# Performance work log

Hardware: AMD Instinct MI355X
Metric: run time of the kernel (lower is better)

Reference implementation:

```python
import jax, jax.numpy as jnp
import numpy as np

DN = ('NCDHW', 'OIDHW', 'NCDHW')

def conv(x, w, stride=1):
    k = w.shape[-1]
    pad = 'VALID' if k == 2 else 'SAME'  # ks=2,s=2 Minkowski offsets {0,1}; ks=3 centered; ks=1 pointwise
    return jax.lax.conv_general_dilated(x, w, (stride,) * 3, pad, dimension_numbers=DN)

def masked_bn(x, m, eps=1e-5):
    # BatchNorm over occupied voxels only (MinkowskiBatchNorm semantics); affine is identity at init.
    cnt = jnp.maximum(jnp.sum(m), 1.0)
    mean = jnp.sum(x * m, axis=(0, 2, 3, 4)) / cnt
    xc = (x - mean.reshape(1, -1, 1, 1, 1)) * m  # also zeroes unoccupied sites
    var = jnp.sum(xc * xc, axis=(0, 2, 3, 4)) / cnt
    return xc * jax.lax.rsqrt(var + eps).reshape(1, -1, 1, 1, 1)

def downmask(m):
    B, _, D, H, W = m.shape
    return m.reshape(B, 1, D // 2, 2, H // 2, 2, W // 2, 2).max(axis=(3, 5, 7))

def cbr(x, m, w):
    return jax.nn.relu(masked_bn(conv(x, w), m))

def res(x, m, wa, wb, wsk):
    y = masked_bn(conv(jax.nn.relu(masked_bn(conv(x, wa), m)), wb), m)
    sk = x if wsk is None else masked_bn(conv(x, wsk), m)
    return jax.nn.relu(y + sk)

def stage(x, m, wd, wa1, wb1, wsk, wa2, wb2):
    m2 = downmask(m)  # output coord set of ks=2,s=2 sparse conv
    x = jax.nn.relu(masked_bn(conv(x, wd, 2), m2))  # BasicConvolutionBlock
    x = res(x, m2, wa1, wb1, wsk)
    x = res(x, m2, wa2, wb2, None)
    return x, m2

def _forward(feats, mask, ws0, ws1, d1, a11, b11, a12, b12, d2, a21, b21, k2, a22, b22,
             d3, a31, b31, k3, a32, b32, d4, a41, b41, k4, a42, b42):
    m = mask
    x = cbr(feats * m, m, ws0)
    x = cbr(x, m, ws1)
    x, m = stage(x, m, d1, a11, b11, None, a12, b12)   # 32 -> 32 (identity skip)
    x, m = stage(x, m, d2, a21, b21, k2, a22, b22)     # 32 -> 64
    x, m = stage(x, m, d3, a31, b31, k3, a32, b32)     # 64 -> 128
    x, m = stage(x, m, d4, a41, b41, k4, a42, b42)     # 128 -> 256
    return x

def setup_inputs() -> dict:
    key = jax.random.key(0)
    ks = jax.random.split(key, 28)
    def W(k, o, i, s):
        return jax.random.normal(k, (o, i, s, s, s), jnp.float32) / np.sqrt(i * s ** 3)
    feats = jax.random.normal(ks[0], (2, 3, 64, 64, 64), jnp.float32)
    mask = (jax.random.uniform(ks[1], (2, 1, 64, 64, 64)) < 0.1).astype(jnp.float32)
    return dict(
        feats=feats * mask, mask=mask,
        ws0=W(ks[2], 32, 3, 3), ws1=W(ks[3], 32, 32, 3),
        d1=W(ks[4], 32, 32, 2), a11=W(ks[5], 32, 32, 3), b11=W(ks[6], 32, 32, 3),
        a12=W(ks[7], 32, 32, 3), b12=W(ks[8], 32, 32, 3),
        d2=W(ks[9], 32, 32, 2), a21=W(ks[10], 64, 32, 3), b21=W(ks[11], 64, 64, 3),
        k2=W(ks[12], 64, 32, 1), a22=W(ks[13], 64, 64, 3), b22=W(ks[14], 64, 64, 3),
        d3=W(ks[15], 64, 64, 2), a31=W(ks[16], 128, 64, 3), b31=W(ks[17], 128, 128, 3),
        k3=W(ks[18], 128, 64, 1), a32=W(ks[19], 128, 128, 3), b32=W(ks[20], 128, 128, 3),
        d4=W(ks[21], 128, 128, 2), a41=W(ks[22], 256, 128, 3), b41=W(ks[23], 256, 256, 3),
        k4=W(ks[24], 256, 128, 1), a42=W(ks[25], 256, 256, 3), b42=W(ks[26], 256, 256, 3))

def reference(feats, mask, ws0, ws1, d1, a11, b11, a12, b12, d2, a21, b21, k2, a22, b22,
              d3, a31, b31, k3, a32, b32, d4, a41, b41, k4, a42, b42):
    return _forward(feats, mask, ws0, ws1, d1, a11, b11, a12, b12, d2, a21, b21, k2, a22, b22,
                    d3, a31, b31, k3, a32, b32, d4, a41, b41, k4, a42, b42)
```

## Files before the change

### kernel.cpp

```cpp
#include <hip/hip_runtime.h>

#define BLK 256

static inline int gup(long work) { return (int)((work + BLK - 1) / BLK); }

__device__ inline bool occ_pred(const float* mask, const int* fmap,
                                int i, int DHW, int Ho, int Wo, int mode) {
  if (mode == 0) return mask[i] > 0.f;
  int b = i / DHW, sp = i - b * DHW;
  int HW = Ho * Wo;
  int z = sp / HW, r = sp - z * HW, y = r / Wo, x = r - y * Wo;
  int Hi = 2 * Ho, Wi = 2 * Wo;
  const int* mb = fmap + b * 8 * DHW;
  int base = ((2 * z) * Hi + 2 * y) * Wi + 2 * x;
  bool occ = false;
  for (int dz = 0; dz < 2; dz++)
    for (int dy = 0; dy < 2; dy++)
      for (int dx = 0; dx < 2; dx++)
        occ |= mb[base + dz * Hi * Wi + dy * Wi + dx] >= 0;
  return occ;
}

__global__ __launch_bounds__(1024) void cnt_k(const float* mask, const int* fmap,
    int* bcnt, int DHW, int Ho, int Wo, int mode, int total) {
  int i = blockIdx.x * 1024 + threadIdx.x;
  bool occ = (i < total) && occ_pred(mask, fmap, i, DHW, Ho, Wo, mode);
  unsigned long long bal = __ballot(occ);
  __shared__ int ws[16];
  int lane = threadIdx.x & 63, wid = threadIdx.x >> 6;
  if (lane == 0) ws[wid] = __popcll(bal);
  __syncthreads();
  if (threadIdx.x == 0) {
    int a = 0;
    for (int w = 0; w < 16; w++) a += ws[w];
    bcnt[blockIdx.x] = a;
  }
}

__global__ __launch_bounds__(1024) void scan_k(int* bcnt, int nb, int* cnt) {
  __shared__ int sh[1024];
  int t = threadIdx.x;
  int v = (t < nb) ? bcnt[t] : 0;
  sh[t] = v;
  __syncthreads();
  for (int o = 1; o < 1024; o <<= 1) {
    int u = (t >= o) ? sh[t - o] : 0;
    __syncthreads();
    sh[t] += u;
    __syncthreads();
  }
  if (t < nb) bcnt[t] = sh[t] - v;
  if (t == 0) *cnt = sh[1023];
}

__global__ __launch_bounds__(1024) void emit_k(const float* mask, const int* fmap,
    const int* boff, int* map, int* list, int DHW, int Ho, int Wo, int mode, int total) {
  int i = blockIdx.x * 1024 + threadIdx.x;
  bool occ = (i < total) && occ_pred(mask, fmap, i, DHW, Ho, Wo, mode);
  unsigned long long bal = __ballot(occ);
  int lane = threadIdx.x & 63, wid = threadIdx.x >> 6;
  __shared__ int wcnt[16], woff[16];
  if (lane == 0) wcnt[wid] = __popcll(bal);
  __syncthreads();
  if (threadIdx.x == 0) {
    int a = boff[blockIdx.x];
    for (int w = 0; w < 16; w++) { woff[w] = a; a += wcnt[w]; }
  }
  __syncthreads();
  if (i < total) {
    if (occ) {
      int p = woff[wid] + __popcll(bal & ((1ull << lane) - 1ull));
      map[i] = p; list[p] = i;
    } else map[i] = -1;
  }
}

__global__ __launch_bounds__(1024) void compact1_k(const int* __restrict__ fmap,
    int* __restrict__ map, int* __restrict__ list, int* __restrict__ cntp,
    int Do, int Ho, int Wo) {
  int DHW = Do * Ho * Wo, total = 2 * DHW;
  int tid = threadIdx.x, lane = tid & 63, wid = tid >> 6;
  bool occ = (tid < total) && occ_pred(nullptr, fmap, tid, DHW, Ho, Wo, 1);
  unsigned long long bal = __ballot(occ);
  __shared__ int wcnt[16], woff[16];
  if (lane == 0) wcnt[wid] = __popcll(bal);
  __syncthreads();
  if (tid == 0) {
    int a = 0;
    for (int w = 0; w < 16; w++) { woff[w] = a; a += wcnt[w]; }
    *cntp = a;
  }
  __syncthreads();
  if (tid < total) {
    if (occ) {
      int p = woff[wid] + __popcll(bal & ((1ull << lane) - 1ull));
      map[tid] = p; list[p] = tid;
    } else map[tid] = -1;
  }
}

__global__ __launch_bounds__(256) void csr_both_k(
    const int* __restrict__ list, const int* __restrict__ map,
    const int* __restrict__ cntp, const int* __restrict__ fmap,
    int* __restrict__ csr27, int* __restrict__ csr8,
    int D, int H, int W, int do8) {
  int n = *cntp;
  int DHW = D * H * W;
  for (int v = blockIdx.x * 256 + threadIdx.x; v < n; v += gridDim.x * 256) {
    int idx = list[v];
    int b = idx / DHW, sp = idx - b * DHW;
    int z = sp / (H * W), r = sp - z * H * W, y = r / W, x = r - y * W;
    const int* mb = map + b * DHW;
    int* e = csr27 + (long)v * 28;
    int cnt = 0;
    for (int k = 0; k < 27; k++) {
      int dz = k / 9 - 1, dy = (k / 3) % 3 - 1, dx = k % 3 - 1;
      int zz = z + dz, yy = y + dy, xx = x + dx;
      if ((unsigned)zz >= (unsigned)D || (unsigned)yy >= (unsigned)H ||
          (unsigned)xx >= (unsigned)W) continue;
      int j = mb[(zz * H + yy) * W + xx];
      if (j >= 0) e[++cnt] = (k << 24) | j;
    }
    e[0] = cnt;
    for (int s = cnt + 1; s <= 27; s++) e[s] = -1;
    if (do8) {
      int Hi = 2 * H, Wi = 2 * W;
      const int* fb = fmap + b * 8 * DHW;
      int* e8 = csr8 + (long)v * 9;
      int c8 = 0;
      for (int k = 0; k < 8; k++) {
        int dz = k >> 2, dy = (k >> 1) & 1, dx = k & 1;
        int j = fb[((2 * z + dz) * Hi + 2 * y + dy) * Wi + 2 * x + dx];
        if (j >= 0) e8[++c8] = (k << 24) | j;
      }
      e8[0] = c8;
      for (int s = c8 + 1; s <= 8; s++) e8[s] = -1;
    }
  }
}

struct WAll {
  const float* src[25];
  float* dst[25];
  int O[25], I[25], K[25];
  int sb[26];
};

__global__ __launch_bounds__(256) void wtr_all_k(WAll wa) {
  int b = blockIdx.x;
  int w = 0;
  while (w < 24 && b >= wa.sb[w + 1]) ++w;
  int O = wa.O[w], I = wa.I[w], K = wa.K[w];
  int I4 = (I + 3) >> 2;
  long tot = (long)K * I4 * O * 4;
  long t = (long)(b - wa.sb[w]) * 256 + threadIdx.x;
  if (t >= tot) return;
  int e = (int)(t & 3); long r = t >> 2;
  int co = (int)(r % O); long r2 = r / O;
  int ci4 = (int)(r2 % I4); int k = (int)(r2 / I4);
  int ci = 4 * ci4 + e;
  wa.dst[w][t] = (ci < I) ? wa.src[w][((long)co * I + ci) * K + k] : 0.f;
}

__global__ void gather0_k(const float* __restrict__ feats, const int* __restrict__ list,
                          const int* __restrict__ cntp, float* __restrict__ rows, int DHW) {
  int n = *cntp;
  int t = blockIdx.x * BLK + threadIdx.x;
  if (t >= n * 4) return;
  int vox = t >> 2, c = t & 3;
  int idx = list[vox]; int b = idx / DHW, sp = idx - b * DHW;
  rows[t] = (c < 3) ? feats[(b * 3 + c) * DHW + sp] : 0.f;
}

template <int CIN, int COUT, int CPT, int VX, int NT, bool PRE>
__global__ __launch_bounds__(256) void convk_k(
    const float* __restrict__ fin, const float* __restrict__ wt,
    float* __restrict__ fout, const int* __restrict__ csr,
    const int* __restrict__ cntp, const int* __restrict__ pcntp,
    const float* __restrict__ pslot, float* __restrict__ slot) {
  constexpr int CL = COUT / CPT;
  constexpr int G = 256 / CL;
  constexpr int VT = G * VX;
  constexpr int C4 = CIN / 4;
  constexpr int WSZ = C4 * COUT;
  __shared__ int jtab[VT * NT];
  __shared__ float4 rbuf[VT * C4];
  __shared__ float4 wbuf[WSZ];
  __shared__ float aP[PRE ? CIN : 4], bP[PRE ? CIN : 4];
  __shared__ float swA[256], swB[256];
  int n = *cntp;
  int vb = blockIdx.x * VT;
  if (vb >= n) return;
  int tid = threadIdx.x;
  if constexpr (PRE) {
    int np = *pcntp;
    float c = fmaxf((float)np, 1.f);
    for (int ch = tid; ch < CIN; ch += 256) {
      float s = 0.f, q = 0.f;
      #pragma unroll
      for (int r = 0; r < 4; r++) { s += pslot[r * 512 + ch]; q += pslot[r * 512 + 256 + ch]; }
      float mean = s / c, var = fmaxf(q / c - mean * mean, 0.f);
      float a = rsqrtf(var + 1e-5f);
      aP[ch] = a; bP[ch] = -mean * a;
    }
  }
  for (int u = tid; u < VT * NT; u += 256) jtab[u] = -1;
  __syncthreads();
  for (int u = tid; u < VT * (NT + 1); u += 256) {
    int v = u / (NT + 1), s = u - v * (NT + 1);
    if (s > 0 && vb + v < n) {
      int e = csr[(long)(vb + v) * (NT + 1) + s];
      if (e >= 0) jtab[v * NT + (e >> 24)] = e & 0xFFFFFF;
    }
  }
  int cl = tid % CL, g = tid / CL, vg = g * VX;
  float acc[VX][CPT];
  #pragma unroll
  for (int vx = 0; vx < VX; vx++)
    #pragma unroll
    for (int m = 0; m < CPT; m++) acc[vx][m] = 0.f;
  const float4* fin4 = (const float4*)fin;
  const float4* w4 = (const float4*)wt;
  for (int k = 0; k < NT; k++) {
    __syncthreads();
    for (int u = tid; u < WSZ; u += 256) wbuf[u] = w4[(long)k * WSZ + u];
    for (int u = tid; u < VT * C4; u += 256) {
      int v = u / C4, c4 = u - v * C4;
      int j = jtab[v * NT + k];
      float4 val = make_float4(0.f, 0.f, 0.f, 0.f);
      if (j >= 0) {
        val = fin4[(long)j * C4 + c4];
        if constexpr (PRE) {
          int ch = 4 * c4;
          val.x = fmaxf(val.x * aP[ch] + bP[ch], 0.f);
          val.y = fmaxf(val.y * aP[ch + 1] + bP[ch + 1], 0.f);
          val.z = fmaxf(val.z * aP[ch + 2] + bP[ch + 2], 0.f);
          val.w = fmaxf(val.w * aP[ch + 3] + bP[ch + 3], 0.f);
        }
      }
      rbuf[u] = val;
    }
    __syncthreads();
    #pragma unroll
    for (int c4 = 0; c4 < C4; c4++) {
      float4 w_[CPT];
      #pragma unroll
      for (int m = 0; m < CPT; m++) w_[m] = wbuf[c4 * COUT + cl + m * CL];
      #pragma unroll
      for (int vx = 0; vx < VX; vx++) {
        float4 rv = rbuf[(vg + vx) * C4 + c4];
        #pragma unroll
        for (int m = 0; m < CPT; m++)
          acc[vx][m] += rv.x * w_[m].x + rv.y * w_[m].y + rv.z * w_[m].z + rv.w * w_[m].w;
      }
    }
  }
  #pragma unroll
  for (int vx = 0; vx < VX; vx++) {
    int v = vb + vg + vx;
    if (v < n) {
      #pragma unroll
      for (int m = 0; m < CPT; m++)
        fout[(long)v * COUT + cl + m * CL] = acc[vx][m];
    }
  }
  int lane = tid & 63, wid = tid >> 6;
  #pragma unroll
  for (int m = 0; m < CPT; m++) {
    float ps = 0.f, pq = 0.f;
    #pragma unroll
    for (int vx = 0; vx < VX; vx++) { ps += acc[vx][m]; pq += acc[vx][m] * acc[vx][m]; }
    #pragma unroll
    for (int o = 32; o >= CL; o >>= 1) {
      ps += __shfl_down(ps, o);
      pq += __shfl_down(pq, o);
    }
    if (lane < CL) {
      swA[(m * 4 + wid) * CL + lane] = ps;
      swB[(m * 4 + wid) * CL + lane] = pq;
    }
  }
  __syncthreads();
  if (tid < COUT) {
    int m = tid / CL, c2 = tid % CL;
    float s = 0.f, q = 0.f;
    #pragma unroll
    for (int w = 0; w < 4; w++) {
      s += swA[(m * 4 + w) * CL + c2];
      q += swB[(m * 4 + w) * CL + c2];
    }
    float* sl = slot + (blockIdx.x & 3) * 512;
    atomicAdd(&sl[tid], s);
    atomicAdd(&sl[256 + tid], q);
  }
}

template <int CIN, int COUT, int ES, bool PRE>
__global__ __launch_bounds__(256) void convc_k(
    const float* __restrict__ fin, const float* __restrict__ wt,
    float* __restrict__ fout, const int* __restrict__ csr,
    const int* __restrict__ cntp, const int* __restrict__ pcntp,
    const float* __restrict__ pslot, float* __restrict__ slot) {
  constexpr int CL = COUT / 2, G = 256 / CL, C4 = CIN / 4;
  constexpr int EST = (ES > 0) ? ES : 1;
  constexpr int CPD = PRE ? CIN : 4;
  __shared__ float4 rbuf[G * C4];
  __shared__ int se[G * EST];
  __shared__ float aP[CPD], bP[CPD];
  __shared__ float sA[256], sB[256];
  __shared__ int scmax;
  int n = *cntp;
  int vb = blockIdx.x * G;
  if (vb >= n) return;
  int tid = threadIdx.x;
  if constexpr (PRE) {
    int np = *pcntp;
    float c = fmaxf((float)np, 1.f);
    for (int ch = tid; ch < CIN; ch += 256) {
      float s = 0.f, q = 0.f;
      #pragma unroll
      for (int r = 0; r < 4; r++) { s += pslot[r * 512 + ch]; q += pslot[r * 512 + 256 + ch]; }
      float mean = s / c, var = fmaxf(q / c - mean * mean, 0.f);
      float a = rsqrtf(var + 1e-5f);
      aP[ch] = a; bP[ch] = -mean * a;
    }
  }
  int cmax;
  if constexpr (ES > 0) {
    if (tid == 0) scmax = 0;
    __syncthreads();
    for (int u = tid; u < G * ES; u += 256) {
      int v = vb + u / ES;
      int e = (v < n) ? csr[(long)vb * ES + u] : 0;
      se[u] = e;
      if ((u % ES) == 0) atomicMax(&scmax, e);
    }
    __syncthreads();
    cmax = scmax;
  } else {
    __syncthreads();
    cmax = 1;
  }
  int cl = tid % CL, g = tid / CL;
  int v = vb + g;
  bool alive = v < n;
  float a0 = 0.f, a1 = 0.f;
  const float4* fin4 = (const float4*)fin;
  const float4* w4 = (const float4*)wt;
  for (int i = 1; i <= cmax; i++) {
    __syncthreads();
    for (int u = tid; u < G * C4; u += 256) {
      int gg = u / C4, c4 = u - gg * C4;
      int pj = -1;
      if constexpr (ES > 0) {
        if (vb + gg < n && i <= se[gg * EST]) pj = se[gg * EST + i];
      } else {
        if (vb + gg < n) pj = vb + gg;
      }
      float4 val = make_float4(0.f, 0.f, 0.f, 0.f);
      if (pj >= 0) {
        int j = pj & 0xFFFFFF;
        val = fin4[(long)j * C4 + c4];
        if constexpr (PRE) {
          int ch = 4 * c4;
          val.x = fmaxf(val.x * aP[ch] + bP[ch], 0.f);
          val.y = fmaxf(val.y * aP[ch + 1] + bP[ch + 1], 0.f);
          val.z = fmaxf(val.z * aP[ch + 2] + bP[ch + 2], 0.f);
          val.w = fmaxf(val.w * aP[ch + 3] + bP[ch + 3], 0.f);
        }
      }
      rbuf[u] = val;
    }
    __syncthreads();
    int pj;
    if constexpr (ES > 0) {
      pj = (alive && i <= se[g * EST]) ? se[g * EST + i] : -1;
    } else {
      pj = alive ? v : -1;
    }
    if (pj >= 0) {
      int k = pj >> 24;
      const float4* wk = w4 + (long)k * C4 * COUT + cl;
      #pragma unroll 8
      for (int c4 = 0; c4 < C4; c4++) {
        float4 rv = rbuf[g * C4 + c4];
        float4 w0 = wk[c4 * COUT];
        float4 w1 = wk[c4 * COUT + CL];
        a0 += rv.x * w0.x + rv.y * w0.y + rv.z * w0.z + rv.w * w0.w;
        a1 += rv.x * w1.x + rv.y * w1.y + rv.z * w1.z + rv.w * w1.w;
      }
    }
  }
  if (alive) {
    fout[(long)v * COUT + cl] = a0;
    fout[(long)v * COUT + cl + CL] = a1;
  }
  __syncthreads();
  sA[tid] = alive ? a0 : 0.f; sB[tid] = alive ? a1 : 0.f;
  __syncthreads();
  for (int o = 128; o >= CL; o >>= 1) {
    if (tid < o) { sA[tid] += sA[tid + o]; sB[tid] += sB[tid + o]; }
    __syncthreads();
  }
  float s0 = 0.f, s1 = 0.f;
  if (tid < CL) { s0 = sA[tid]; s1 = sB[tid]; }
  __syncthreads();
  sA[tid] = alive ? a0 * a0 : 0.f; sB[tid] = alive ? a1 * a1 : 0.f;
  __syncthreads();
  for (int o = 128; o >= CL; o >>= 1) {
    if (tid < o) { sA[tid] += sA[tid + o]; sB[tid] += sB[tid + o]; }
    __syncthreads();
  }
  if (tid < CL) {
    float* sl = slot + (blockIdx.x & 3) * 512;
    atomicAdd(&sl[tid], s0);
    atomicAdd(&sl[tid + CL], s1);
    atomicAdd(&sl[256 + tid], sA[tid]);
    atomicAdd(&sl[256 + tid + CL], sB[tid]);
  }
}

template <int CIN, int COUT, int NS, bool PRE>
__global__ __launch_bounds__(256) void convs_k(
    const float* __restrict__ fin, const float* __restrict__ wt,
    float* __restrict__ fout, const int* __restrict__ csr,
    const int* __restrict__ cntp, const int* __restrict__ pcntp,
    const float* __restrict__ pslot) {
  constexpr int CL = COUT / 2, G = 256 / CL, C4 = CIN / 4;
  constexpr int CPD = PRE ? CIN : 4;
  __shared__ float4 rbuf[G * C4];
  __shared__ int se[G * 28];
  __shared__ float aP[CPD], bP[CPD];
  __shared__ int scmax;
  int n = *cntp;
  int vb = blockIdx.x * G;
  if (vb >= n) return;
  int tid = threadIdx.x;
  int y = blockIdx.y;
  if constexpr (PRE) {
    int np = *pcntp;
    float c = fmaxf((float)np, 1.f);
    for (int ch = tid; ch < CIN; ch += 256) {
      float s = 0.f, q = 0.f;
      #pragma unroll
      for (int r = 0; r < 4; r++) { s += pslot[r * 512 + ch]; q += pslot[r * 512 + 256 + ch]; }
      float mean = s / c, var = fmaxf(q / c - mean * mean, 0.f);
      float a = rsqrtf(var + 1e-5f);
      aP[ch] = a; bP[ch] = -mean * a;
    }
  }
  if (tid == 0) scmax = 0;
  __syncthreads();
  for (int u = tid; u < G * 28; u += 256) {
    int v = vb + u / 28;
    int e = (v < n) ? csr[(long)vb * 28 + u] : 0;
    se[u] = e;
    if ((u % 28) == 0) atomicMax(&scmax, e);
  }
  __syncthreads();
  int cmax = scmax;
  int cl = tid % CL, g = tid / CL;
  int v = vb + g;
  bool alive = v < n;
  float a0 = 0.f, a1 = 0.f;
  const float4* fin4 = (const float4*)fin;
  const float4* w4 = (const float4*)wt;
  for (int i = 1 + y; i <= cmax; i += NS) {
    __syncthreads();
    for (int u = tid; u < G * C4; u += 256) {
      int gg = u / C4, c4 = u - gg * C4;
      int pj = -1;
      if (vb + gg < n && i <= se[gg * 28]) pj = se[gg * 28 + i];
      float4 val = make_float4(0.f, 0.f, 0.f, 0.f);
      if (pj >= 0) {
        int j = pj & 0xFFFFFF;
        val = fin4[(long)j * C4 + c4];
        if constexpr (PRE) {
          int ch = 4 * c4;
          val.x = fmaxf(val.x * aP[ch] + bP[ch], 0.f);
          val.y = fmaxf(val.y * aP[ch + 1] + bP[ch + 1], 0.f);
          val.z = fmaxf(val.z * aP[ch + 2] + bP[ch + 2], 0.f);
          val.w = fmaxf(val.w * aP[ch + 3] + bP[ch + 3], 0.f);
        }
      }
      rbuf[u] = val;
    }
    __syncthreads();
    int pj = (alive && i <= se[g * 28]) ? se[g * 28 + i] : -1;
    if (pj >= 0) {
      int k = pj >> 24;
      const float4* wk = w4 + (long)k * C4 * COUT + cl;
      #pragma unroll 8
      for (int c4 = 0; c4 < C4; c4++) {
        float4 rv = rbuf[g * C4 + c4];
        float4 w0 = wk[c4 * COUT];
        float4 w1 = wk[c4 * COUT + CL];
        a0 += rv.x * w0.x + rv.y * w0.y + rv.z * w0.z + rv.w * w0.w;
        a1 += rv.x * w1.x + rv.y * w1.y + rv.z * w1.z + rv.w * w1.w;
      }
    }
  }
  if (alive) {
    atomicAdd(&fout[(long)v * COUT + cl], a0);
    atomicAdd(&fout[(long)v * COUT + cl + CL], a1);
  }
}

template <int C>
__global__ __launch_bounds__(BLK) void bnred_k(const float* __restrict__ rows,
    const int* __restrict__ cntp, float* __restrict__ slot) {
  int n = *cntp;
  long tot = (long)n * C;
  int tid = threadIdx.x;
  float s = 0.f, s2 = 0.f;
  for (long t = (long)blockIdx.x * BLK + tid; t < tot; t += (long)gridDim.x * BLK) {
    float v = rows[t]; s += v; s2 += v * v;
  }
  __shared__ float sh[BLK], sh2[BLK];
  sh[tid] = s; sh2[tid] = s2;
  __syncthreads();
  for (int o = BLK / 2; o >= C; o >>= 1) {
    if (tid < o) { sh[tid] += sh[tid + o]; sh2[tid] += sh2[tid + o]; }
    __syncthreads();
  }
  if (tid < C) { atomicAdd(&slot[tid], sh[tid]); atomicAdd(&slot[256 + tid], sh2[tid]); }
}

template <int C, int MODE>
__global__ __launch_bounds__(256) void skipapp_k(
    const float* __restrict__ x, const float* __restrict__ y,
    const float* __restrict__ s1, const float* __restrict__ s2,
    const int* __restrict__ cntp, float* __restrict__ out) {
  __shared__ float a1_[C], b1_[C], a2_[C], b2_[C];
  int n = *cntp;
  int tid = threadIdx.x;
  float cnt = fmaxf((float)n, 1.f);
  for (int c = tid; c < C; c += 256) {
    float s = 0.f, q = 0.f;
    #pragma unroll
    for (int r = 0; r < 4; r++) { s += s1[r * 512 + c]; q += s1[r * 512 + 256 + c]; }
    float mean = s / cnt, var = fmaxf(q / cnt - mean * mean, 0.f);
    float a = rsqrtf(var + 1e-5f);
    a1_[c] = a; b1_[c] = -mean * a;
    if (MODE != 2) {
      s = 0.f; q = 0.f;
      #pragma unroll
      for (int r = 0; r < 4; r++) { s += s2[r * 512 + c]; q += s2[r * 512 + 256 + c]; }
      mean = s / cnt; var = fmaxf(q / cnt - mean * mean, 0.f);
      a = rsqrtf(var + 1e-5f);
      a2_[c] = a; b2_[c] = -mean * a;
    }
  }
  __syncthreads();
  constexpr int C4 = C / 4;
  long tot = (long)n * C4;
  for (long t = (long)blockIdx.x * 256 + tid; t < tot; t += (long)gridDim.x * 256) {
    int c = 4 * (int)(t % C4);
    float4 xv = ((const float4*)x)[t];
    float4 yv = ((const float4*)y)[t];
    float4 o;
    o.x = xv.x * a1_[c] + b1_[c];
    o.y = xv.y * a1_[c + 1] + b1_[c + 1];
    o.z = xv.z * a1_[c + 2] + b1_[c + 2];
    o.w = xv.w * a1_[c + 3] + b1_[c + 3];
    if (MODE == 0) {
      o.x += yv.x * a2_[c] + b2_[c];
      o.y += yv.y * a2_[c + 1] + b2_[c + 1];
      o.z += yv.z * a2_[c + 2] + b2_[c + 2];
      o.w += yv.w * a2_[c + 3] + b2_[c + 3];
    } else if (MODE == 1) {
      o.x += fmaxf(yv.x * a2_[c] + b2_[c], 0.f);
      o.y += fmaxf(yv.y * a2_[c + 1] + b2_[c + 1], 0.f);
      o.z += fmaxf(yv.z * a2_[c + 2] + b2_[c + 2], 0.f);
      o.w += fmaxf(yv.w * a2_[c + 3] + b2_[c + 3], 0.f);
    } else {
      o.x += yv.x; o.y += yv.y; o.z += yv.z; o.w += yv.w;
    }
    o.x = fmaxf(o.x, 0.f); o.y = fmaxf(o.y, 0.f);
    o.z = fmaxf(o.z, 0.f); o.w = fmaxf(o.w, 0.f);
    ((float4*)out)[t] = o;
  }
}

__global__ void scatter_k(const float* __restrict__ rows, const int* __restrict__ list,
                          const int* __restrict__ cntp, float* __restrict__ out, int DHW) {
  int n = *cntp;
  int t = blockIdx.x * BLK + threadIdx.x;
  if (t >= n * 256) return;
  int vox = t >> 8, c = t & 255;
  int idx = list[vox]; int b = idx / DHW, sp = idx - b * DHW;
  out[(b * 256 + c) * DHW + sp] = rows[t];
}

#define CAP0 81920
#define CAP1 57344
#define CAP2 8192
#define CAP3 1024
#define CAP4 128

extern "C" void kernel_launch(void* const* d_in, const int* in_sizes, int n_in,
                              void* d_out, int out_size, void* d_ws, size_t ws_size,
                              hipStream_t stream) {
  const float* feats = (const float*)d_in[0];
  const float* mask0 = (const float*)d_in[1];

  char* p = (char*)d_ws;
  auto alloc = [&](size_t bytes) { char* r = p; p += (bytes + 255) & ~255ull; return r; };

  const int tab[25][4] = {
    {2, 32, 3, 27},  {3, 32, 32, 27}, {4, 32, 32, 8},  {5, 32, 32, 27}, {6, 32, 32, 27},
    {7, 32, 32, 27}, {8, 32, 32, 27}, {9, 32, 32, 8},  {10, 64, 32, 27},{11, 64, 64, 27},
    {12, 64, 32, 1}, {13, 64, 64, 27},{14, 64, 64, 27},{15, 64, 64, 8}, {16, 128, 64, 27},
    {17, 128, 128, 27},{18, 128, 64, 1},{19, 128, 128, 27},{20, 128, 128, 27},
    {21, 128, 128, 8},{22, 256, 128, 27},{23, 256, 256, 27},{24, 256, 128, 1},
    {25, 256, 256, 27},{26, 256, 256, 27},
  };
  WAll wa;
  float* wT[27] = {nullptr};
  int blk = 0;
  for (int i = 0; i < 25; i++) {
    int idx = tab[i][0], O = tab[i][1], I = tab[i][2], K = tab[i][3];
    int I4 = (I + 3) / 4;
    long sz = (long)K * I4 * O * 4;
    wT[idx] = (float*)alloc((size_t)sz * 4);
    wa.src[i] = (const float*)d_in[idx]; wa.dst[i] = wT[idx];
    wa.O[i] = O; wa.I[i] = I; wa.K[i] = K;
    wa.sb[i] = blk; blk += (int)((sz + 255) / 256);
  }
  wa.sb[25] = blk;

  int* map0 = (int*)alloc(524288 * 4);
  int* list0 = (int*)alloc((size_t)CAP0 * 4);
  int* map1 = (int*)alloc(65536 * 4);
  int* list1 = (int*)alloc((size_t)CAP1 * 4);
  int* map2 = (int*)alloc(8192 * 4);
  int* list2 = (int*)alloc(8192 * 4);
  int* map3 = (int*)alloc(1024 * 4);
  int* list3 = (int*)alloc(1024 * 4);
  int* map4 = (int*)alloc(128 * 4);
  int* list4 = (int*)alloc(128 * 4);
  int* bcnt = (int*)alloc(1024 * 4);
  int* cnts = (int*)alloc(32 * 4);
  int* c27_0 = (int*)alloc((size_t)CAP0 * 28 * 4);
  int* c27_1 = (int*)alloc((size_t)CAP1 * 28 * 4);
  int* c8_1  = (int*)alloc((size_t)CAP1 * 9 * 4);
  int* c27_2 = (int*)alloc((size_t)CAP2 * 28 * 4);
  int* c8_2  = (int*)alloc((size_t)CAP2 * 9 * 4);
  int* c27_3 = (int*)alloc((size_t)CAP3 * 28 * 4);
  int* c8_3  = (int*)alloc((size_t)CAP3 * 9 * 4);
  int* c27_4 = (int*)alloc((size_t)CAP4 * 28 * 4);
  int* c8_4  = (int*)alloc((size_t)CAP4 * 9 * 4);
  float* stats = (float*)alloc(25 * 2048 * 4);
  float* G0  = (float*)alloc((size_t)CAP0 * 4 * 4);
  float* F0a = (float*)alloc((size_t)CAP0 * 32 * 4);
  float* F0b = (float*)alloc((size_t)CAP0 * 32 * 4);
  float *R1[4], *R2[4];
  for (int i = 0; i < 4; i++) R1[i] = (float*)alloc((size_t)CAP1 * 32 * 4);
  for (int i = 0; i < 4; i++) R2[i] = (float*)alloc((size_t)CAP2 * 64 * 4);
  size_t z3sz = (size_t)CAP3 * 128 * 4 * 6 + (size_t)CAP4 * 256 * 4 * 6;
  float* Z3 = (float*)alloc(z3sz);
  float* R3[6], *R4[6];
  for (int i = 0; i < 6; i++) R3[i] = Z3 + (size_t)i * CAP3 * 128;
  for (int i = 0; i < 6; i++) R4[i] = Z3 + (size_t)6 * CAP3 * 128 + (size_t)i * CAP4 * 256;

  hipMemsetAsync(stats, 0, 25 * 2048 * 4, stream);
  hipMemsetAsync(Z3, 0, z3sz, stream);
  hipMemsetAsync(d_out, 0, (size_t)out_size * 4, stream);

  wtr_all_k<<<blk, 256, 0, stream>>>(wa);

  int* n0 = cnts + 0; int* n1 = cnts + 1; int* n2 = cnts + 2;
  int* n3 = cnts + 3; int* n4 = cnts + 4;

  cnt_k<<<512, 1024, 0, stream>>>(mask0, nullptr, bcnt, 262144, 64, 64, 0, 524288);
  scan_k<<<1, 1024, 0, stream>>>(bcnt, 512, n0);
  emit_k<<<512, 1024, 0, stream>>>(mask0, nullptr, bcnt, map0, list0, 262144, 64, 64, 0, 524288);
  gather0_k<<<gup((long)CAP0 * 4), BLK, 0, stream>>>(feats, list0, n0, G0, 262144);
  csr_both_k<<<512, 256, 0, stream>>>(list0, map0, n0, nullptr, c27_0, nullptr, 64, 64, 64, 0);

  cnt_k<<<64, 1024, 0, stream>>>(nullptr, map0, bcnt, 32768, 32, 32, 1, 65536);
  scan_k<<<1, 1024, 0, stream>>>(bcnt, 64, n1);
  emit_k<<<64, 1024, 0, stream>>>(nullptr, map0, bcnt, map1, list1, 32768, 32, 32, 1, 65536);
  csr_both_k<<<256, 256, 0, stream>>>(list1, map1, n1, map0, c27_1, c8_1, 32, 32, 32, 1);

  cnt_k<<<8, 1024, 0, stream>>>(nullptr, map1, bcnt, 4096, 16, 16, 1, 8192);
  scan_k<<<1, 1024, 0, stream>>>(bcnt, 8, n2);
  emit_k<<<8, 1024, 0, stream>>>(nullptr, map1, bcnt, map2, list2, 4096, 16, 16, 1, 8192);
  csr_both_k<<<32, 256, 0, stream>>>(list2, map2, n2, map1, c27_2, c8_2, 16, 16, 16, 1);

  compact1_k<<<1, 1024, 0, stream>>>(map2, map3, list3, n3, 8, 8, 8);
  csr_both_k<<<4, 256, 0, stream>>>(list3, map3, n3, map2, c27_3, c8_3, 8, 8, 8, 1);

  compact1_k<<<1, 1024, 0, stream>>>(map3, map4, list4, n4, 4, 4, 4);
  csr_both_k<<<1, 256, 0, stream>>>(list4, map4, n4, map3, c27_4, c8_4, 4, 4, 4, 1);

  auto slot = [&](int i) { return stats + (size_t)i * 2048; };
  auto bgrid = [&](long cap, int C) { long g = (cap * C / 4 + 255) / 256; return (int)(g > 2048 ? 2048 : g); };

  {
    int g = (CAP0 + 63) / 64;
    convk_k<4, 32, 4, 2, 27, false><<<g, 256, 0, stream>>>(G0, wT[2], F0a, c27_0, n0, nullptr, nullptr, slot(0));
    convk_k<32, 32, 4, 2, 27, true><<<g, 256, 0, stream>>>(F0a, wT[3], F0b, c27_0, n0, n0, slot(0), slot(1));
  }

  {
    int g = (CAP1 + 63) / 64, ag = bgrid(CAP1, 32);
    convk_k<32, 32, 4, 2, 8, true><<<g, 256, 0, stream>>>(F0b, wT[4], R1[0], c8_1, n1, n0, slot(1), slot(2));
    convk_k<32, 32, 4, 2, 27, true><<<g, 256, 0, stream>>>(R1[0], wT[5], R1[1], c27_1, n1, n1, slot(2), slot(3));
    convk_k<32, 32, 4, 2, 27, true><<<g, 256, 0, stream>>>(R1[1], wT[6], R1[2], c27_1, n1, n1, slot(3), slot(4));
    skipapp_k<32, 1><<<ag, 256, 0, stream>>>(R1[2], R1[0], slot(4), slot(2), n1, R1[3]);
    convk_k<32, 32, 4, 2, 27, false><<<g, 256, 0, stream>>>(R1[3], wT[7], R1[1], c27_1, n1, nullptr, nullptr, slot(5));
    convk_k<32, 32, 4, 2, 27, true><<<g, 256, 0, stream>>>(R1[1], wT[8], R1[2], c27_1, n1, n1, slot(5), slot(6));
    skipapp_k<32, 2><<<ag, 256, 0, stream>>>(R1[2], R1[3], slot(6), nullptr, n1, R1[0]);
  }

  {
    int g32 = (CAP2 + 31) / 32, ag = bgrid(CAP2, 64);
    convk_k<32, 32, 4, 1, 8, false><<<g32, 256, 0, stream>>>(R1[0], wT[9], R2[0], c8_2, n2, nullptr, nullptr, slot(7));
    convk_k<32, 64, 4, 2, 27, true><<<g32, 256, 0, stream>>>(R2[0], wT[10], R2[1], c27_2, n2, n2, slot(7), slot(8));
    convk_k<64, 64, 4, 2, 27, true><<<g32, 256, 0, stream>>>(R2[1], wT[11], R2[2], c27_2, n2, n2, slot(8), slot(9));
    convc_k<32, 64, 0, true><<<(CAP2 + 7) / 8, 256, 0, stream>>>(R2[0], wT[12], R2[3], nullptr, n2, n2, slot(7), slot(10));
    skipapp_k<64, 0><<<ag, 256, 0, stream>>>(R2[2], R2[3], slot(9), slot(10), n2, R2[1]);
    convk_k<64, 64, 4, 2, 27, false><<<g32, 256, 0, stream>>>(R2[1], wT[13], R2[0], c27_2, n2, nullptr, nullptr, slot(11));
    convk_k<64, 64, 4, 2, 27, true><<<g32, 256, 0, stream>>>(R2[0], wT[14], R2[2], c27_2, n2, n2, slot(11), slot(12));
    skipapp_k<64, 2><<<ag, 256, 0, stream>>>(R2[2], R2[1], slot(12), nullptr, n2, R2[3]);
  }

  {
    int gP = (CAP3 + 7) / 8, gO = (CAP3 + 3) / 4, ag = bgrid(CAP3, 128);
    int rO = gup((long)CAP3 * 128); if (rO > 512) rO = 512;
    convc_k<64, 64, 9, false><<<gP, 256, 0, stream>>>(R2[3], wT[15], R3[0], c8_3, n3, nullptr, nullptr, slot(13));
    convs_k<64, 128, 4, true><<<dim3(gO, 4), 256, 0, stream>>>(R3[0], wT[16], R3[1], c27_3, n3, n3, slot(13));
    bnred_k<128><<<rO, BLK, 0, stream>>>(R3[1], n3, slot(14));
    convs_k<128, 128, 4, true><<<dim3(gO, 4), 256, 0, stream>>>(R3[1], wT[17], R3[2], c27_3, n3, n3, slot(14));
    bnred_k<128><<<rO, BLK, 0, stream>>>(R3[2], n3, slot(15));
    convc_k<64, 128, 0, true><<<gO, 256, 0, stream>>>(R3[0], wT[18], R3[3], nullptr, n3, n3, slot(13), slot(16));
    skipapp_k<128, 0><<<ag, 256, 0, stream>>>(R3[2], R3[3], slot(15), slot(16), n3, R3[1]);
    convs_k<128, 128, 4, false><<<dim3(gO, 4), 256, 0, stream>>>(R3[1], wT[19], R3[4], c27_3, n3, nullptr, nullptr);
    bnred_k<128><<<rO, BLK, 0, stream>>>(R3[4], n3, slot(17));
    convs_k<128, 128, 4, true><<<dim3(gO, 4), 256, 0, stream>>>(R3[4], wT[20], R3[5], c27_3, n3, n3, slot(17));
    bnred_k<128><<<rO, BLK, 0, stream>>>(R3[5], n3, slot(18));
    skipapp_k<128, 2><<<ag, 256, 0, stream>>>(R3[5], R3[1], slot(18), nullptr, n3, R3[0]);
  }

  {
    int gP = (CAP4 + 3) / 4, gO = (CAP4 + 1) / 2, ag = bgrid(CAP4, 256);
    int rO = gup((long)CAP4 * 256); if (rO > 512) rO = 512;
    convc_k<128, 128, 9, false><<<gP, 256, 0, stream>>>(R3[0], wT[21], R4[0], c8_4, n4, nullptr, nullptr, slot(19));
    convs_k<128, 256, 16, true><<<dim3(gO, 16), 256, 0, stream>>>(R4[0], wT[22], R4[1], c27_4, n4, n4, slot(19));
    bnred_k<256><<<rO, BLK, 0, stream>>>(R4[1], n4, slot(20));
    convs_k<256, 256, 16, true><<<dim3(gO, 16), 256, 0, stream>>>(R4[1], wT[23], R4[2], c27_4, n4, n4, slot(20));
    bnred_k<256><<<rO, BLK, 0, stream>>>(R4[2], n4, slot(21));
    convc_k<128, 256, 0, true><<<gO, 256, 0, stream>>>(R4[0], wT[24], R4[3], nullptr, n4, n4, slot(19), slot(22));
    skipapp_k<256, 0><<<ag, 256, 0, stream>>>(R4[2], R4[3], slot(21), slot(22), n4, R4[1]);
    convs_k<256, 256, 16, false><<<dim3(gO, 16), 256, 0, stream>>>(R4[1], wT[25], R4[4], c27_4, n4, nullptr, nullptr);
    bnred_k<256><<<rO, BLK, 0, stream>>>(R4[4], n4, slot(23));
    convs_k<256, 256, 16, true><<<dim3(gO, 16), 256, 0, stream>>>(R4[4], wT[26], R4[5], c27_4, n4, n4, slot(23));
    bnred_k<256><<<rO, BLK, 0, stream>>>(R4[5], n4, slot(24));
    skipapp_k<256, 2><<<ag, 256, 0, stream>>>(R4[5], R4[1], slot(24), nullptr, n4, R4[0]);
  }

  scatter_k<<<gup((long)CAP4 * 256), BLK, 0, stream>>>(R4[0], list4, n4, (float*)d_out, 64);
}
```

Before: 1.499 ms.

## Replace per-voxel sparse conv with weight-tiled kernel-offset-split conv for stages 3-4

Adds convw_k, which builds a per-block table mapping each voxel to its neighbour for every kernel offset. It stages each active offset's weight tile and the gathered input rows in shared memory, so weights are reused across 16 voxels instead of being read from global memory per voxel. Work is split across output-channel tiles and kernel-offset groups, with partial sums combined through atomicAdd. It also pads the rbuf row stride to avoid LDS bank conflicts in convk_k. The risk is extra atomic traffic, and the grid size CAP/16 assumes CAP is divisible by 16.

Result: no change. 1.498 ms (-0.0%).

```diff
diff --git a/kernel.cpp b/kernel.cpp
--- a/kernel.cpp
+++ b/kernel.cpp
@@ -182,9 +182,10 @@
   constexpr int G = 256 / CL;
   constexpr int VT = G * VX;
   constexpr int C4 = CIN / 4;
+  constexpr int RST = C4 + 1;
   constexpr int WSZ = C4 * COUT;
   __shared__ int jtab[VT * NT];
-  __shared__ float4 rbuf[VT * C4];
+  __shared__ float4 rbuf[VT * RST];
   __shared__ float4 wbuf[WSZ];
   __shared__ float aP[PRE ? CIN : 4], bP[PRE ? CIN : 4];
   __shared__ float swA[256], swB[256];
@@ -238,7 +239,7 @@
           val.w = fmaxf(val.w * aP[ch + 3] + bP[ch + 3], 0.f);
         }
       }
-      rbuf[u] = val;
+      rbuf[v * RST + c4] = val;
     }
     __syncthreads();
     #pragma unroll
@@ -248,7 +249,7 @@
       for (int m = 0; m < CPT; m++) w_[m] = wbuf[c4 * COUT + cl + m * CL];
       #pragma unroll
       for (int vx = 0; vx < VX; vx++) {
-        float4 rv = rbuf[(vg + vx) * C4 + c4];
+        float4 rv = rbuf[(vg + vx) * RST + c4];
         #pragma unroll
         for (int m = 0; m < CPT; m++)
           acc[vx][m] += rv.x * w_[m].x + rv.y * w_[m].y + rv.z * w_[m].z + rv.w * w_[m].w;
@@ -292,6 +293,106 @@
     float* sl = slot + (blockIdx.x & 3) * 512;
     atomicAdd(&sl[tid], s);
     atomicAdd(&sl[256 + tid], q);
+  }
+}
+
+template <int CIN, int COUT, int COT, int VT, int KSP, bool PRE>
+__global__ __launch_bounds__(256) void convw_k(
+    const float* __restrict__ fin, const float* __restrict__ wt,
+    float* __restrict__ fout, const int* __restrict__ csr,
+    const int* __restrict__ cntp, const int* __restrict__ pcntp,
+    const float* __restrict__ pslot) {
+  constexpr int CL = COT / 2;
+  constexpr int G = 256 / CL;
+  constexpr int VX = VT / G;
+  constexpr int C4 = CIN / 4;
+  constexpr int RST = C4 + 1;
+  __shared__ float4 wbuf[C4 * COT];
+  __shared__ float4 rbuf[VT * RST];
+  __shared__ int jt[VT * 27];
+  __shared__ int act[27];
+  __shared__ float aP[PRE ? CIN : 4], bP[PRE ? CIN : 4];
+  int n = *cntp;
+  int vb = blockIdx.x * VT;
+  if (vb >= n) return;
+  int tid = threadIdx.x;
+  int c0 = blockIdx.y * COT;
+  if constexpr (PRE) {
+    int np = *pcntp;
+    float c = fmaxf((float)np, 1.f);
+    for (int ch = tid; ch < CIN; ch += 256) {
+      float s = 0.f, q = 0.f;
+      #pragma unroll
+      for (int r = 0; r < 4; r++) { s += pslot[r * 512 + ch]; q += pslot[r * 512 + 256 + ch]; }
+      float mean = s / c, var = fmaxf(q / c - mean * mean, 0.f);
+      float a = rsqrtf(var + 1e-5f);
+      aP[ch] = a; bP[ch] = -mean * a;
+    }
+  }
+  if (tid < 27) act[tid] = 0;
+  for (int u = tid; u < VT * 27; u += 256) jt[u] = -1;
+  __syncthreads();
+  for (int u = tid; u < VT * 28; u += 256) {
+    int v = u / 28, s = u - v * 28;
+    if (s > 0 && vb + v < n) {
+      int e = csr[(long)(vb + v) * 28 + s];
+      if (e >= 0) {
+        int k = e >> 24;
+        jt[v * 27 + k] = e & 0xFFFFFF;
+        atomicOr(&act[k], 1);
+      }
+    }
+  }
+  __syncthreads();
+  int cl = tid % CL, g = tid / CL, vg = g * VX;
+  float acc[VX][2];
+  #pragma unroll
+  for (int vx = 0; vx < VX; vx++) { acc[vx][0] = 0.f; acc[vx][1] = 0.f; }
+  const float4* fin4 = (const float4*)fin;
+  const float4* w4 = (const float4*)wt;
+  for (int k = blockIdx.z; k < 27; k += KSP) {
+    if (!act[k]) continue;
+    __syncthreads();
+    for (int u = tid; u < C4 * COT; u += 256) {
+      int ci4 = u / COT, co = u - ci4 * COT;
+      wbuf[u] = w4[(long)k * C4 * COUT + ci4 * COUT + c0 + co];
+    }
+    for (int u = tid; u < VT * C4; u += 256) {
+      int v = u / C4, c4 = u - v * C4;
+      int j = jt[v * 27 + k];
+      float4 val = make_float4(0.f, 0.f, 0.f, 0.f);
+      if (j >= 0) {
+        val = fin4[(long)j * C4 + c4];
+        if constexpr (PRE) {
+          int ch = 4 * c4;
+          val.x = fmaxf(val.x * aP[ch] + bP[ch], 0.f);
+          val.y = fmaxf(val.y * aP[ch + 1] + bP[ch + 1], 0.f);
+          val.z = fmaxf(val.z * aP[ch + 2] + bP[ch + 2], 0.f);
+          val.w = fmaxf(val.w * aP[ch + 3] + bP[ch + 3], 0.f);
+        }
+      }
+      rbuf[v * RST + c4] = val;
+    }
+    __syncthreads();
+    #pragma unroll 8
+    for (int c4 = 0; c4 < C4; c4++) {
+      float4 w0 = wbuf[c4 * COT + cl];
+      float4 w1 = wbuf[c4 * COT + cl + CL];
+      #pragma unroll
+      for (int vx = 0; vx < VX; vx++) {
+        float4 rv = rbuf[(vg + vx) * RST + c4];
+        acc[vx][0] += rv.x * w0.x + rv.y * w0.y + rv.z * w0.z + rv.w * w0.w;
+        acc[vx][1] += rv.x * w1.x + rv.y * w1.y + rv.z * w1.z + rv.w * w1.w;
+      }
+    }
+  }
+  #pragma unroll
+  for (int vx = 0; vx < VX; vx++) {
+    int v = vb + vg + vx;
+    if (v < n) {
+      atomicAdd(&fout[(long)v * COUT + c0 + cl], acc[vx][0]);
+      atomicAdd(&fout[(long)v * COUT + c0 + cl + CL], acc[vx][1]);
+    }
   }
 }
 
@@ -417,92 +518,6 @@
     atomicAdd(&sl[tid + CL], s1);
     atomicAdd(&sl[256 + tid], sA[tid]);
     atomicAdd(&sl[256 + tid + CL], sB[tid]);
-  }
-}
-
-template <int CIN, int COUT, int NS, bool PRE>
-__global__ __launch_bounds__(256) void convs_k(
-    const float* __restrict__ fin, const float* __restrict__ wt,
-    float* __restrict__ fout, const int* __restrict__ csr,
-    const int* __restrict__ cntp, const int* __restrict__ pcntp,
-    const float* __restrict__ pslot) {
-  constexpr int CL = COUT / 2, G = 256 / CL, C4 = CIN / 4;
-  constexpr int CPD = PRE ? CIN : 4;
-  __shared__ float4 rbuf[G * C4];
-  __shared__ int se[G * 28];
-  __shared__ float aP[CPD], bP[CPD];
-  __shared__ int scmax;
-  int n = *cntp;
-  int vb = blockIdx.x * G;
-  if (vb >= n) return;
-  int tid = threadIdx.x;
-  int y = blockIdx.y;
-  if constexpr (PRE) {
-    int np = *pcntp;
-    float c = fmaxf((float)np, 1.f);
-    for (int ch = tid; ch < CIN; ch += 256) {
-      float s = 0.f, q = 0.f;
-      #pragma unroll
-      for (int r = 0; r < 4; r++) { s += pslot[r * 512 + ch]; q += pslot[r * 512 + 256 + ch]; }
-      float mean = s / c, var = fmaxf(q / c - mean * mean, 0.f);
-      float a = rsqrtf(var + 1e-5f);
-      aP[ch] = a; bP[ch] = -mean * a;
-    }
-  }
-  if (tid == 0) scmax = 0;
-  __syncthreads();
-  for (int u = tid; u < G * 28; u += 256) {
-    int v = vb + u / 28;
-    int e = (v < n) ? csr[(long)vb * 28 + u] : 0;
-    se[u] = e;
-    if ((u % 28) == 0) atomicMax(&scmax, e);
-  }
-  __syncthreads();
-  int cmax = scmax;
-  int cl = tid % CL, g = tid / CL;
-  int v = vb + g;
-  bool alive = v < n;
-  float a0 = 0.f, a1 = 0.f;
-  const float4* fin4 = (const float4*)fin;
-  const float4* w4 = (const float4*)wt;
-  for (int i = 1 + y; i <= cmax; i += NS) {
-    __syncthreads();
-    for (int u = tid; u < G * C4; u += 256) {
-      int gg = u / C4, c4 = u - gg * C4;
-      int pj = -1;
-      if (vb + gg < n && i <= se[gg * 28]) pj = se[gg * 28 + i];
-      float4 val = make_float4(0.f, 0.f, 0.f, 0.f);
-      if (pj >= 0) {
-        int j = pj & 0xFFFFFF;
-        val = fin4[(long)j * C4 + c4];
-        if constexpr (PRE) {
-          int ch = 4 * c4;
-          val.x = fmaxf(val.x * aP[ch] + bP[ch], 0.f);
-          val.y = fmaxf(val.y * aP[ch + 1] + bP[ch + 1], 0.f);
-          val.z = fmaxf(val.z * aP[ch + 2] + bP[ch + 2], 0.f);
-          val.w = fmaxf(val.w * aP[ch + 3] + bP[ch + 3], 0.f);
-        }
-      }
-      rbuf[u] = val;
-    }
-    __syncthreads();
-    int pj = (alive && i <= se[g * 28]) ? se[g * 28 + i] : -1;
-    if (pj >= 0) {
-      int k = pj >> 24;
-      const float4* wk = w4 + (long)k * C4 * COUT + cl;
-      #pragma unroll 8
-      for (int c4 = 0; c4 < C4; c4++) {
-        float4 rv = rbuf[g * C4 + c4];
-        float4 w0 = wk[c4 * COUT];
-        float4 w1 = wk[c4 * COUT + CL];
-        a0 += rv.x * w0.x + rv.y * w0.y + rv.z * w0.z + rv.w * w0.w;
-        a1 += rv.x * w1.x + rv.y * w1.y + rv.z * w1.z + rv.w * w1.w;
-      }
-    }
-  }
-  if (alive) {
-    atomicAdd(&fout[(long)v * COUT + cl], a0);
-    atomicAdd(&fout[(long)v * COUT + cl + CL], a1);
   }
 }
 
@@ -729,16 +744,17 @@
   {
     int gP = (CAP3 + 7) / 8, gO = (CAP3 + 3) / 4, ag = bgrid(CAP3, 128);
     int rO = gup((long)CAP3 * 128); if (rO > 512) rO = 512;
+    dim3 gw(CAP3 / 16, 1, 4);
     convc_k<64, 64, 9, false><<<gP, 256, 0, stream>>>(R2[3], wT[15], R3[0], c8_3, n3, nullptr, nullptr, slot(13));
-    convs_k<64, 128, 4, true><<<dim3(gO, 4), 256, 0, stream>>>(R3[0], wT[16], R3[1], c27_3, n3, n3, slot(13));
+    convw_k<64, 128, 128, 16, 4, true><<<gw, 256, 0, stream>>>(R3[0], wT[16], R3[1], c27_3, n3, n3, slot(13));
     bnred_k<128><<<rO, BLK, 0, stream>>>(R3[1], n3, slot(14));
-    convs_k<128, 128, 4, true><<<dim3(gO, 4), 256, 0, stream>>>(R3[1], wT[17], R3[2], c27_3, n3, n3, slot(14));
+    convw_k<128, 128, 128, 16, 4, true><<<gw, 256, 0, stream>>>(R3[1], wT[17], R3[2], c27_3, n3, n3, slot(14));
     bnred_k<128><<<rO, BLK, 0, stream>>>(R3[2], n3, slot(15));
     convc_k<64, 128, 0, true><<<gO, 256, 0, stream>>>(R3[0], wT[18], R3[3], nullptr, n3, n3, slot(13), slot(16));
     skipapp_k<128, 0><<<ag, 256, 0, stream>>>(R3[2], R3[3], slot(15), slot(16), n3, R3[1]);
-    convs_k<128, 128, 4, false><<<dim3(gO, 4), 256, 0, stream>>>(R3[1], wT[19], R3[4], c27_3, n3, nullptr, nullptr);
+    convw_k<128, 128, 128, 16, 4, false><<<gw, 256, 0, stream>>>(R3[1], wT[19], R3[4], c27_3, n3, nullptr, nullptr);
     bnred_k<128><<<rO, BLK, 0, stream>>>(R3[4], n3, slot(17));
-    convs_k<128, 128, 4, true><<<dim3(gO, 4), 256, 0, stream>>>(R3[4], wT[20], R3[5], c27_3, n3, n3, slot(17));
+    convw_k<128, 128, 128, 16, 4, true><<<gw, 256, 0, stream>>>(R3[4], wT[20], R3[5], c27_3, n3, n3, slot(17));
     bnred_k<128><<<rO, BLK, 0, stream>>>(R3[5], n3, slot(18));
     skipapp_k<128, 2><<<ag, 256, 0, stream>>>(R3[5], R3[1], slot(18), nullptr, n3, R3[0]);
   }
@@ -746,16 +762,17 @@
   {
     int gP = (CAP4 + 3) / 4, gO = (CAP4 + 1) / 2, ag = bgrid(CAP4, 256);
     int rO = gup((long)CAP4 * 256); if (rO > 512) rO = 512;
+    dim3 gw(CAP4 / 16, 4, 8);
     convc_k<128, 128, 9, false><<<gP, 256, 0, stream>>>(R3[0], wT[21], R4[0], c8_4, n4, nullptr, nullptr, slot(19));
-    convs_k<128, 256, 16, true><<<dim3(gO, 16), 256, 0, stream>>>(R4[0], wT[22], R4[1], c27_4, n4, n4, slot(19));
+    convw_k<128, 256, 64, 16, 8, true><<<gw, 256, 0, stream>>>(R4[0], wT[22], R4[1], c27_4, n4, n4, slot(19));
     bnred_k<256><<<rO, BLK, 0, stream>>>(R4[1], n4, slot(20));
-    convs_k<256, 256, 16, true><<<dim3(gO, 16), 256, 0, stream>>>(R4[1], wT[23], R4[2], c27_4, n4, n4, slot(20));
+    convw_k<256, 256, 64, 16, 8, true><<<gw, 256, 0, stream>>>(R4[1], wT[23], R4[2], c27_4, n4, n4, slot(20));
     bnred_k<256><<<rO, BLK, 0, stream>>>(R4[2], n4, slot(21));
     convc_k<128, 256, 0, true><<<gO, 256, 0, stream>>>(R4[0], wT[24], R4[3], nullptr, n4, n4, slot(19), slot(22));
     skipapp_k<256, 0><<<ag, 256, 0, stream>>>(R4[2], R4[3], slot(21), slot(22), n4, R4[1]);
-    convs_k<256, 256, 16, false><<<dim3(gO, 16), 256, 0, stream>>>(R4[1], wT[25], R4[4], c27_4, n4, nullptr, nullptr);
+    convw_k<256, 256, 64, 16, 8, false><<<gw, 256, 0, stream>>>(R4[1], wT[25], R4[4], c27_4, n4, nullptr, nullptr);
     bnred_k<256><<<rO, BLK, 0, stream>>>(R4[4], n4, slot(23));
-    convs_k<256, 256, 16, true><<<dim3(gO, 16), 256, 0, stream>>>(R4[4], wT[26], R4[5], c27_4, n4, n4, slot(23));
+    convw_k<256, 256, 64, 16, 8, true><<<gw, 256, 0, stream>>>(R4[4], wT[26], R4[5], c27_4, n4, n4, slot(23));
     bnred_k<256><<<rO, BLK, 0, stream>>>(R4[5], n4, slot(24));
     skipapp_k<256, 2><<<ag, 256, 0, stream>>>(R4[5], R4[1], slot(24), nullptr, n4, R4[0]);
   }
```
